# Performance work log

Hardware: AMD Instinct MI355X
Metric: run time of the kernel (lower is better)

Reference implementation:

```python
import jax, jax.numpy as jnp
import numpy as np


def _tet_geometry(vertices, indices, tet_density):
    """Gather 4 corners per tet, compute area (|det|/6), min edge length, alpha."""
    v = vertices[indices]                      # [T,4,3]
    v0, v1, v2, v3 = v[:, 0], v[:, 1], v[:, 2], v[:, 3]
    # --- tet area: |det([v1-v0, v2-v0, v3-v0])| / 6 ---
    e1, e2, e3 = v1 - v0, v2 - v0, v3 - v0     # [T,3] each
    det = (e1[:, 0] * (e2[:, 1] * e3[:, 2] - e2[:, 2] * e3[:, 1])
           - e1[:, 1] * (e2[:, 0] * e3[:, 2] - e2[:, 2] * e3[:, 0])
           + e1[:, 2] * (e2[:, 0] * e3[:, 1] - e2[:, 1] * e3[:, 0]))
    tet_area = jnp.abs(det) / 6.0              # [T]
    # --- edge lengths of all 6 edges, take min (mode='min') ---
    edge_sq = jnp.stack([
        jnp.sum((v0 - v1) ** 2, axis=1),
        jnp.sum((v0 - v2) ** 2, axis=1),
        jnp.sum((v0 - v3) ** 2, axis=1),
        jnp.sum((v1 - v2) ** 2, axis=1),
        jnp.sum((v1 - v3) ** 2, axis=1),
        jnp.sum((v2 - v3) ** 2, axis=1),
    ], axis=0)                                 # [6,T]
    el = jnp.sqrt(jnp.min(edge_sq, axis=0))    # [T]
    tet_alpha = 1.0 - jnp.exp(-tet_density * el)
    return tet_area, tet_alpha


def _vert_density(tet_density, indices, num_verts):
    # torch scatter_reduce_ 'amax' with zero-initialized dest and include_self=True
    # == segment_max over all 4 corner slots, clamped below at 0.
    flat_idx = indices.reshape(-1)                         # [4T]
    src = jnp.repeat(tet_density, 4)                       # [4T], matches row-major flatten
    vmax = jax.ops.segment_max(src, flat_idx, num_segments=num_verts)
    return jnp.maximum(vmax, jnp.zeros((), vmax.dtype))    # untouched verts -> 0


def setup_inputs() -> dict:
    key = jax.random.key(0)
    k1, k2, k3 = jax.random.split(key, 3)
    V, T = 1_000_000, 4_000_000
    vertices = jax.random.normal(k1, (V, 3), dtype=jnp.float32)
    indices = jax.random.randint(k2, (T, 4), 0, V, dtype=jnp.int32)
    tet_density = jax.random.uniform(k3, (T,), dtype=jnp.float32)
    return {"vertices": vertices, "indices": indices, "tet_density": tet_density}


def reference(vertices, indices, tet_density):
    tet_area, tet_alpha = _tet_geometry(vertices, indices, tet_density)
    vert_density = _vert_density(tet_density, indices, vertices.shape[0])
    return tet_area, tet_alpha, vert_density
```

## Files before the change

kernel.cpp:

```cpp
#include <hip/hip_runtime.h>

typedef int nt_int4 __attribute__((ext_vector_type(4)));

#define NB     256
#define VSHIFT 12
#define BMASK  ((1 << VSHIFT) - 1)
#define BCAP   65536
#define RT     4
#define NR     4

__global__ __launch_bounds__(256) void zero_kernel(uint4* __restrict__ vd4, int n4,
                                                   unsigned* __restrict__ gcnt) {
    int i = blockIdx.x * blockDim.x + threadIdx.x;
    if (i < n4) vd4[i] = make_uint4(0u, 0u, 0u, 0u);
    if (gcnt && i < NB) gcnt[i] = 0u;
}

__global__ __launch_bounds__(256) void pad_verts_kernel(const float* __restrict__ verts,
                                                        float4* __restrict__ verts4, int V) {
    int i = blockIdx.x * blockDim.x + threadIdx.x;
    if (i < V) {
        const float* p = verts + (size_t)i * 3;
        verts4[i] = make_float4(p[0], p[1], p[2], 0.f);
    }
}

__global__ __launch_bounds__(256) void geom_kernel_v4(
    const float4* __restrict__ verts4,
    const int*   __restrict__ indices,
    const float* __restrict__ density,
    float* __restrict__ out_area,
    float* __restrict__ out_alpha,
    int T)
{
    int i = blockIdx.x * blockDim.x + threadIdx.x;
    if (i >= T) return;

    nt_int4 idx = __builtin_nontemporal_load((const nt_int4*)indices + i);
    float d     = __builtin_nontemporal_load(&density[i]);

    float4 v0 = verts4[idx.x];
    float4 v1 = verts4[idx.y];
    float4 v2 = verts4[idx.z];
    float4 v3 = verts4[idx.w];

    float e1x = v1.x - v0.x, e1y = v1.y - v0.y, e1z = v1.z - v0.z;
    float e2x = v2.x - v0.x, e2y = v2.y - v0.y, e2z = v2.z - v0.z;
    float e3x = v3.x - v0.x, e3y = v3.y - v0.y, e3z = v3.z - v0.z;

    float det = e1x * (e2y * e3z - e2z * e3y)
              - e1y * (e2x * e3z - e2z * e3x)
              + e1z * (e2x * e3y - e2y * e3x);
    __builtin_nontemporal_store(fabsf(det) * (1.0f / 6.0f), &out_area[i]);

    float q01 = e1x * e1x + e1y * e1y + e1z * e1z;
    float q02 = e2x * e2x + e2y * e2y + e2z * e2z;
    float q03 = e3x * e3x + e3y * e3y + e3z * e3z;
    float ax, ay, az;
    ax = v1.x - v2.x; ay = v1.y - v2.y; az = v1.z - v2.z;
    float q12 = ax * ax + ay * ay + az * az;
    ax = v1.x - v3.x; ay = v1.y - v3.y; az = v1.z - v3.z;
    float q13 = ax * ax + ay * ay + az * az;
    ax = v2.x - v3.x; ay = v2.y - v3.y; az = v2.z - v3.z;
    float q23 = ax * ax + ay * ay + az * az;

    float mn = fminf(fminf(fminf(q01, q02), fminf(q03, q12)), fminf(q13, q23));
    float el = sqrtf(mn);
    __builtin_nontemporal_store(1.0f - expf(-d * el), &out_alpha[i]);
}

__global__ __launch_bounds__(256) void geom_kernel_raw(
    const float* __restrict__ verts,
    const int*   __restrict__ indices,
    const float* __restrict__ density,
    float* __restrict__ out_area,
    float* __restrict__ out_alpha,
    int T)
{
    int i = blockIdx.x * blockDim.x + threadIdx.x;
    if (i >= T) return;

    nt_int4 idx = __builtin_nontemporal_load((const nt_int4*)indices + i);
    float d     = __builtin_nontemporal_load(&density[i]);

    const float* p;
    p = verts + (size_t)idx.x * 3; float v0x = p[0], v0y = p[1], v0z = p[2];
    p = verts + (size_t)idx.y * 3; float v1x = p[0], v1y = p[1], v1z = p[2];
    p = verts + (size_t)idx.z * 3; float v2x = p[0], v2y = p[1], v2z = p[2];
    p = verts + (size_t)idx.w * 3; float v3x = p[0], v3y = p[1], v3z = p[2];

    float e1x = v1x - v0x, e1y = v1y - v0y, e1z = v1z - v0z;
    float e2x = v2x - v0x, e2y = v2y - v0y, e2z = v2z - v0z;
    float e3x = v3x - v0x, e3y = v3y - v0y, e3z = v3z - v0z;

    float det = e1x * (e2y * e3z - e2z * e3y)
              - e1y * (e2x * e3z - e2z * e3x)
              + e1z * (e2x * e3y - e2y * e3x);
    __builtin_nontemporal_store(fabsf(det) * (1.0f / 6.0f), &out_area[i]);

    float q01 = e1x * e1x + e1y * e1y + e1z * e1z;
    float q02 = e2x * e2x + e2y * e2y + e2z * e2z;
    float q03 = e3x * e3x + e3y * e3y + e3z * e3z;
    float ax, ay, az;
    ax = v1x - v2x; ay = v1y - v2y; az = v1z - v2z;
    float q12 = ax * ax + ay * ay + az * az;
    ax = v1x - v3x; ay = v1y - v3y; az = v1z - v3z;
    float q13 = ax * ax + ay * ay + az * az;
    ax = v2x - v3x; ay = v2y - v3y; az = v2z - v3z;
    float q23 = ax * ax + ay * ay + az * az;

    float mn = fminf(fminf(fminf(q01, q02), fminf(q03, q12)), fminf(q13, q23));
    float el = sqrtf(mn);
    __builtin_nontemporal_store(1.0f - expf(-d * el), &out_alpha[i]);
}

__global__ __launch_bounds__(256) void bin2_kernel(
    const int4*  __restrict__ idx4,
    const float* __restrict__ dens,
    uint2*       __restrict__ pairs,
    unsigned*    __restrict__ gcnt,
    unsigned*    __restrict__ vd,
    int T)
{
    __shared__ unsigned s_cnt[NB];
    __shared__ unsigned s_run[NB];
    __shared__ unsigned s_roff[NB];
    __shared__ unsigned s_wc[NB];
    __shared__ unsigned s_scan[NB];
    __shared__ uint2    stage[256 * RT * 4];

    int tid  = threadIdx.x;
    int base = blockIdx.x * (256 * RT * NR);

    s_cnt[tid] = 0u;
    __syncthreads();
    for (int k = 0; k < RT * NR; ++k) {
        int i = base + k * 256 + tid;
        if (i < T) {
            int4 q = idx4[i];
            atomicAdd(&s_cnt[(unsigned)q.x >> VSHIFT], 1u);
            atomicAdd(&s_cnt[(unsigned)q.y >> VSHIFT], 1u);
            atomicAdd(&s_cnt[(unsigned)q.z >> VSHIFT], 1u);
            atomicAdd(&s_cnt[(unsigned)q.w >> VSHIFT], 1u);
        }
    }
    __syncthreads();

    s_run[tid] = atomicAdd(&gcnt[tid], s_cnt[tid]);
    __syncthreads();

    for (int r = 0; r < NR; ++r) {
        int4  q[RT];
        float dd[RT];
        bool  vl[RT];
#pragma unroll
        for (int k = 0; k < RT; ++k) {
            int i = base + (r * RT + k) * 256 + tid;
            vl[k] = (i < T);
            if (vl[k]) { q[k] = idx4[i]; dd[k] = dens[i]; }
        }

        s_cnt[tid] = 0u;
        __syncthreads();
#pragma unroll
        for (int k = 0; k < RT; ++k) if (vl[k]) {
            atomicAdd(&s_cnt[(unsigned)q[k].x >> VSHIFT], 1u);
            atomicAdd(&s_cnt[(unsigned)q[k].y >> VSHIFT], 1u);
            atomicAdd(&s_cnt[(unsigned)q[k].z >> VSHIFT], 1u);
            atomicAdd(&s_cnt[(unsigned)q[k].w >> VSHIFT], 1u);
        }
        __syncthreads();

        unsigned x = s_cnt[tid];
        s_scan[tid] = x;
        __syncthreads();
        for (int s = 1; s < NB; s <<= 1) {
            unsigned t = (tid >= s) ? s_scan[tid - s] : 0u;
            __syncthreads();
            s_scan[tid] += t;
            __syncthreads();
        }
        s_roff[tid] = s_scan[tid] - x;
        s_wc[tid]   = 0u;
        __syncthreads();
        unsigned npairs = s_scan[NB - 1];

#pragma unroll
        for (int k = 0; k < RT; ++k) if (vl[k]) {
            unsigned db = __float_as_uint(dd[k]);
            unsigned vv[4] = { (unsigned)q[k].x, (unsigned)q[k].y,
                               (unsigned)q[k].z, (unsigned)q[k].w };
#pragma unroll
            for (int j = 0; j < 4; ++j) {
                unsigned b    = vv[j] >> VSHIFT;
                unsigned slot = s_roff[b] + atomicAdd(&s_wc[b], 1u);
                stage[slot] = make_uint2(vv[j], db);
            }
        }
        __syncthreads();

        for (unsigned l = tid; l < npairs; l += 256) {
            uint2 e = stage[l];
            unsigned b  = e.x >> VSHIFT;
            unsigned rr = s_run[b] + (l - s_roff[b]);
            if (rr < BCAP) pairs[(size_t)b * BCAP + rr] = e;
            else           atomicMax(vd + e.x, e.y);
        }
        __syncthreads();

        s_run[tid] += s_cnt[tid];
        __syncthreads();
    }
}

__global__ __launch_bounds__(1024) void bucket_max_kernel(
    const uint2*    __restrict__ pairs,
    const unsigned* __restrict__ gcnt,
    unsigned*       __restrict__ vd,
    int V)
{
    __shared__ unsigned tbl[1 << VSHIFT];
    int b   = blockIdx.x;
    int tid = threadIdx.x;

    for (int j = tid; j < (1 << VSHIFT); j += 1024) tbl[j] = 0u;
    __syncthreads();

    unsigned cnt = gcnt[b];
    if (cnt > BCAP) cnt = BCAP;
    const uint2* p = pairs + (size_t)b * BCAP;
    for (unsigned i = tid; i < cnt; i += 1024) {
        uint2 e = p[i];
        atomicMax(&tbl[e.x & BMASK], e.y);
    }
    __syncthreads();

    int vbase = b << VSHIFT;
    for (int j = tid; j < (1 << VSHIFT); j += 1024) {
        int v = vbase + j;
        if (v < V) {
            unsigned cur = vd[v];
            unsigned t   = tbl[j];
            vd[v] = cur > t ? cur : t;
        }
    }
}

__global__ __launch_bounds__(256) void tet_kernel_filter(
    const float4* __restrict__ verts4,
    const int*   __restrict__ indices,
    const float* __restrict__ density,
    float* __restrict__ out_area,
    float* __restrict__ out_alpha,
    unsigned int* __restrict__ vd,
    int T)
{
    int i = blockIdx.x * blockDim.x + threadIdx.x;
    if (i >= T) return;

    nt_int4 idx = __builtin_nontemporal_load((const nt_int4*)indices + i);
    float d     = __builtin_nontemporal_load(&density[i]);
    unsigned int db = __float_as_uint(d);

    unsigned int c0 = vd[idx.x];
    unsigned int c1 = vd[idx.y];
    unsigned int c2 = vd[idx.z];
    unsigned int c3 = vd[idx.w];

    float4 v0 = verts4[idx.x];
    float4 v1 = verts4[idx.y];
    float4 v2 = verts4[idx.z];
    float4 v3 = verts4[idx.w];

    float e1x = v1.x - v0.x, e1y = v1.y - v0.y, e1z = v1.z - v0.z;
    float e2x = v2.x - v0.x, e2y = v2.y - v0.y, e2z = v2.z - v0.z;
    float e3x = v3.x - v0.x, e3y = v3.y - v0.y, e3z = v3.z - v0.z;

    float det = e1x * (e2y * e3z - e2z * e3y)
              - e1y * (e2x * e3z - e2z * e3x)
              + e1z * (e2x * e3y - e2y * e3x);
    __builtin_nontemporal_store(fabsf(det) * (1.0f / 6.0f), &out_area[i]);

    float q01 = e1x * e1x + e1y * e1y + e1z * e1z;
    float q02 = e2x * e2x + e2y * e2y + e2z * e2z;
    float q03 = e3x * e3x + e3y * e3y + e3z * e3z;
    float ax, ay, az;
    ax = v1.x - v2.x; ay = v1.y - v2.y; az = v1.z - v2.z;
    float q12 = ax * ax + ay * ay + az * az;
    ax = v1.x - v3.x; ay = v1.y - v3.y; az = v1.z - v3.z;
    float q13 = ax * ax + ay * ay + az * az;
    ax = v2.x - v3.x; ay = v2.y - v3.y; az = v2.z - v3.z;
    float q23 = ax * ax + ay * ay + az * az;

    float mn = fminf(fminf(fminf(q01, q02), fminf(q03, q12)), fminf(q13, q23));
    float el = sqrtf(mn);
    __builtin_nontemporal_store(1.0f - expf(-d * el), &out_alpha[i]);

    if (db > c0) atomicMax(vd + idx.x, db);
    if (db > c1) atomicMax(vd + idx.y, db);
    if (db > c2) atomicMax(vd + idx.z, db);
    if (db > c3) atomicMax(vd + idx.w, db);
}

__global__ __launch_bounds__(256) void tet_kernel_fb(
    const float* __restrict__ verts,
    const int4*  __restrict__ indices,
    const float* __restrict__ density,
    float* __restrict__ out_area,
    float* __restrict__ out_alpha,
    unsigned int* __restrict__ vd,
    int T)
{
    int i = blockIdx.x * blockDim.x + threadIdx.x;
    if (i >= T) return;

    int4 idx = indices[i];
    float d = density[i];

    const float* p;
    p = verts + idx.x * 3; float v0x = p[0], v0y = p[1], v0z = p[2];
    p = verts + idx.y * 3; float v1x = p[0], v1y = p[1], v1z = p[2];
    p = verts + idx.z * 3; float v2x = p[0], v2y = p[1], v2z = p[2];
    p = verts + idx.w * 3; float v3x = p[0], v3y = p[1], v3z = p[2];

    float e1x = v1x - v0x, e1y = v1y - v0y, e1z = v1z - v0z;
    float e2x = v2x - v0x, e2y = v2y - v0y, e2z = v2z - v0z;
    float e3x = v3x - v0x, e3y = v3y - v0y, e3z = v3z - v0z;

    float det = e1x * (e2y * e3z - e2z * e3y)
              - e1y * (e2x * e3z - e2z * e3x)
              + e1z * (e2x * e3y - e2y * e3x);
    out_area[i] = fabsf(det) * (1.0f / 6.0f);

    float q01 = e1x * e1x + e1y * e1y + e1z * e1z;
    float q02 = e2x * e2x + e2y * e2y + e2z * e2z;
    float q03 = e3x * e3x + e3y * e3y + e3z * e3z;
    float ax, ay, az;
    ax = v1x - v2x; ay = v1y - v2y; az = v1z - v2z;
    float q12 = ax * ax + ay * ay + az * az;
    ax = v1x - v3x; ay = v1y - v3y; az = v1z - v3z;
    float q13 = ax * ax + ay * ay + az * az;
    ax = v2x - v3x; ay = v2y - v3y; az = v2z - v3z;
    float q23 = ax * ax + ay * ay + az * az;

    float mn = fminf(fminf(fminf(q01, q02), fminf(q03, q12)), fminf(q13, q23));
    float el = sqrtf(mn);
    out_alpha[i] = 1.0f - expf(-d * el);

    unsigned int db = __float_as_uint(d);
    atomicMax(vd + idx.x, db);
    atomicMax(vd + idx.y, db);
    atomicMax(vd + idx.z, db);
    atomicMax(vd + idx.w, db);
}


extern "C" void kernel_launch(void* const* d_in, const int* in_sizes, int n_in,
                              void* d_out, int out_size, void* d_ws, size_t ws_size,
                              hipStream_t stream) {
    const float* verts   = (const float*)d_in[0];
    const int*   indices = (const int*)d_in[1];
    const float* density = (const float*)d_in[2];
    int T = in_sizes[2];
    int V = in_sizes[0] / 3;

    float* out       = (float*)d_out;
    float* out_area  = out;
    float* out_alpha = out + (size_t)T;
    unsigned int* vd = (unsigned int*)(out + 2 * (size_t)T);

    const int block = 256;
    int n4 = V / 4;

    size_t pairsB = (size_t)NB * BCAP * sizeof(uint2);
    size_t cntB   = (size_t)NB * sizeof(unsigned);
    size_t v4B    = (size_t)V * sizeof(float4);

    double mean = 4.0 * (double)T / NB;
    bool capOK = (mean + 12.0 * __builtin_sqrt(mean) <= (double)BCAP);
    bool fastOK = (V % 4 == 0) && (V <= (NB << VSHIFT)) && capOK && d_ws;

    int tetsPerBlock = block * RT * NR;

    if (fastOK && ws_size >= pairsB + cntB + v4B) {
        uint2*    pairs  = (uint2*)d_ws;
        unsigned* gcnt   = (unsigned*)((char*)d_ws + pairsB);
        float4*   verts4 = (float4*)((char*)d_ws + pairsB + ((cntB + 255) & ~(size_t)255));

        zero_kernel<<<(n4 + block - 1) / block, block, 0, stream>>>((uint4*)vd, n4, gcnt);
        pad_verts_kernel<<<(V + block - 1) / block, block, 0, stream>>>(verts, verts4, V);
        geom_kernel_v4<<<(T + block - 1) / block, block, 0, stream>>>(
            verts4, indices, density, out_area, out_alpha, T);

        bin2_kernel<<<(T + tetsPerBlock - 1) / tetsPerBlock, block, 0, stream>>>(
            (const int4*)indices, density, pairs, gcnt, vd, T);

        int nbAct = (V + (1 << VSHIFT) - 1) >> VSHIFT;
        bucket_max_kernel<<<nbAct, 1024, 0, stream>>>(pairs, gcnt, vd, V);
    } else if (fastOK && ws_size >= pairsB + cntB) {
        uint2*    pairs = (uint2*)d_ws;
        unsigned* gcnt  = (unsigned*)((char*)d_ws + pairsB);

        zero_kernel<<<(n4 + block - 1) / block, block, 0, stream>>>((uint4*)vd, n4, gcnt);
        geom_kernel_raw<<<(T + block - 1) / block, block, 0, stream>>>(
            verts, indices, density, out_area, out_alpha, T);

        bin2_kernel<<<(T + tetsPerBlock - 1) / tetsPerBlock, block, 0, stream>>>(
            (const int4*)indices, density, pairs, gcnt, vd, T);

        int nbAct = (V + (1 << VSHIFT) - 1) >> VSHIFT;
        bucket_max_kernel<<<nbAct, 1024, 0, stream>>>(pairs, gcnt, vd, V);
    } else if (d_ws && ws_size >= v4B && (V % 4) == 0) {
        zero_kernel<<<(n4 + block - 1) / block, block, 0, stream>>>((uint4*)vd, n4, nullptr);
        float4* verts4 = (float4*)d_ws;
        pad_verts_kernel<<<(V + block - 1) / block, block, 0, stream>>>(verts, verts4, V);
        tet_kernel_filter<<<(T + block - 1) / block, block, 0, stream>>>(
            verts4, indices, density, out_area, out_alpha, vd, T);
    } else {
        zero_kernel<<<(n4 + block - 1) / block, block, 0, stream>>>((uint4*)vd, n4, nullptr);
        tet_kernel_fb<<<(T + block - 1) / block, block, 0, stream>>>(
            verts, (const int4*)indices, density, out_area, out_alpha, vd, T);
    }
}
```

Measured before the change: 450.0 us.

## Fuse tet geometry computation into the vertex-density binning kernel

The separate geometry kernel is removed, and its per-tet area and alpha computation now runs inside the binning kernel, reusing the index and density values that kernel already loads. This avoids reading the index and density arrays a second time and drops one launch. The fused kernel is launched with far fewer blocks (each handles 4096 tets) and has more register pressure, so the scattered vertex gathers may get less latency hiding. The fast path that lacked a padded-vertex workspace is also removed, so configurations that hit it now fall through to the filter or fallback paths.

Result: faster. 429.0 us (-4.7%).

```diff
diff --git a/kernel.cpp b/kernel.cpp
--- a/kernel.cpp
+++ b/kernel.cpp
@@ -25,98 +25,12 @@
     }
 }
 
-__global__ __launch_bounds__(256) void geom_kernel_v4(
+__global__ __launch_bounds__(256) void fused_geom_bin_kernel(
     const float4* __restrict__ verts4,
-    const int*   __restrict__ indices,
-    const float* __restrict__ density,
+    const int4*  __restrict__ idx4,
+    const float* __restrict__ dens,
     float* __restrict__ out_area,
     float* __restrict__ out_alpha,
-    int T)
-{
-    int i = blockIdx.x * blockDim.x + threadIdx.x;
-    if (i >= T) return;
-
-    nt_int4 idx = __builtin_nontemporal_load((const nt_int4*)indices + i);
-    float d     = __builtin_nontemporal_load(&density[i]);
-
-    float4 v0 = verts4[idx.x];
-    float4 v1 = verts4[idx.y];
-    float4 v2 = verts4[idx.z];
-    float4 v3 = verts4[idx.w];
-
-    float e1x = v1.x - v0.x, e1y = v1.y - v0.y, e1z = v1.z - v0.z;
-    float e2x = v2.x - v0.x, e2y = v2.y - v0.y, e2z = v2.z - v0.z;
-    float e3x = v3.x - v0.x, e3y = v3.y - v0.y, e3z = v3.z - v0.z;
-
-    float det = e1x * (e2y * e3z - e2z * e3y)
-              - e1y * (e2x * e3z - e2z * e3x)
-              + e1z * (e2x * e3y - e2y * e3x);
-    __builtin_nontemporal_store(fabsf(det) * (1.0f / 6.0f), &out_area[i]);
-
-    float q01 = e1x * e1x + e1y * e1y + e1z * e1z;
-    float q02 = e2x * e2x + e2y * e2y + e2z * e2z;
-    float q03 = e3x * e3x + e3y * e3y + e3z * e3z;
-    float ax, ay, az;
-    ax = v1.x - v2.x; ay = v1.y - v2.y; az = v1.z - v2.z;
-    float q12 = ax * ax + ay * ay + az * az;
-    ax = v1.x - v3.x; ay = v1.y - v3.y; az = v1.z - v3.z;
-    float q13 = ax * ax + ay * ay + az * az;
-    ax = v2.x - v3.x; ay = v2.y - v3.y; az = v2.z - v3.z;
-    float q23 = ax * ax + ay * ay + az * az;
-
-    float mn = fminf(fminf(fminf(q01, q02), fminf(q03, q12)), fminf(q13, q23));
-    float el = sqrtf(mn);
-    __builtin_nontemporal_store(1.0f - expf(-d * el), &out_alpha[i]);
-}
-
-__global__ __launch_bounds__(256) void geom_kernel_raw(
-    const float* __restrict__ verts,
-    const int*   __restrict__ indices,
-    const float* __restrict__ density,
-    float* __restrict__ out_area,
-    float* __restrict__ out_alpha,
-    int T)
-{
-    int i = blockIdx.x * blockDim.x + threadIdx.x;
-    if (i >= T) return;
-
-    nt_int4 idx = __builtin_nontemporal_load((const nt_int4*)indices + i);
-    float d     = __builtin_nontemporal_load(&density[i]);
-
-    const float* p;
-    p = verts + (size_t)idx.x * 3; float v0x = p[0], v0y = p[1], v0z = p[2];
-    p = verts + (size_t)idx.y * 3; float v1x = p[0], v1y = p[1], v1z = p[2];
-    p = verts + (size_t)idx.z * 3; float v2x = p[0], v2y = p[1], v2z = p[2];
-    p = verts + (size_t)idx.w * 3; float v3x = p[0], v3y = p[1], v3z = p[2];
-
-    float e1x = v1x - v0x, e1y = v1y - v0y, e1z = v1z - v0z;
-    float e2x = v2x - v0x, e2y = v2y - v0y, e2z = v2z - v0z;
-    float e3x = v3x - v0x, e3y = v3y - v0y, e3z = v3z - v0z;
-
-    float det = e1x * (e2y * e3z - e2z * e3y)
-              - e1y * (e2x * e3z - e2z * e3x)
-              + e1z * (e2x * e3y - e2y * e3x);
-    __builtin_nontemporal_store(fabsf(det) * (1.0f / 6.0f), &out_area[i]);
-
-    float q01 = e1x * e1x + e1y * e1y + e1z * e1z;
-    float q02 = e2x * e2x + e2y * e2y + e2z * e2z;
-    float q03 = e3x * e3x + e3y * e3y + e3z * e3z;
-    float ax, ay, az;
-    ax = v1x - v2x; ay = v1y - v2y; az = v1z - v2z;
-    float q12 = ax * ax + ay * ay + az * az;
-    ax = v1x - v3x; ay = v1y - v3y; az = v1z - v3z;
-    float q13 = ax * ax + ay * ay + az * az;
-    ax = v2x - v3x; ay = v2y - v3y; az = v2z - v3z;
-    float q23 = ax * ax + ay * ay + az * az;
-
-    float mn = fminf(fminf(fminf(q01, q02), fminf(q03, q12)), fminf(q13, q23));
-    float el = sqrtf(mn);
-    __builtin_nontemporal_store(1.0f - expf(-d * el), &out_alpha[i]);
-}
-
-__global__ __launch_bounds__(256) void bin2_kernel(
-    const int4*  __restrict__ idx4,
-    const float* __restrict__ dens,
     uint2*       __restrict__ pairs,
     unsigned*    __restrict__ gcnt,
     unsigned*    __restrict__ vd,
@@ -160,6 +74,39 @@
             if (vl[k]) { q[k] = idx4[i]; dd[k] = dens[i]; }
         }
 
+#pragma unroll
+        for (int k = 0; k < RT; ++k) if (vl[k]) {
+            int i = base + (r * RT + k) * 256 + tid;
+            float4 v0 = verts4[q[k].x];
+            float4 v1 = verts4[q[k].y];
+            float4 v2 = verts4[q[k].z];
+            float4 v3 = verts4[q[k].w];
+
+            float e1x = v1.x - v0.x, e1y = v1.y - v0.y, e1z = v1.z - v0.z;
+            float e2x = v2.x - v0.x, e2y = v2.y - v0.y, e2z = v2.z - v0.z;
+            float e3x = v3.x - v0.x, e3y = v3.y - v0.y, e3z = v3.z - v0.z;
+
+            float det = e1x * (e2y * e3z - e2z * e3y)
+                      - e1y * (e2x * e3z - e2z * e3x)
+                      + e1z * (e2x * e3y - e2y * e3x);
+            __builtin_nontemporal_store(fabsf(det) * (1.0f / 6.0f), &out_area[i]);
+
+            float q01 = e1x * e1x + e1y * e1y + e1z * e1z;
+            float q02 = e2x * e2x + e2y * e2y + e2z * e2z;
+            float q03 = e3x * e3x + e3y * e3y + e3z * e3z;
+            float ax, ay, az;
+            ax = v1.x - v2.x; ay = v1.y - v2.y; az = v1.z - v2.z;
+            float q12 = ax * ax + ay * ay + az * az;
+            ax = v1.x - v3.x; ay = v1.y - v3.y; az = v1.z - v3.z;
+            float q13 = ax * ax + ay * ay + az * az;
+            ax = v2.x - v3.x; ay = v2.y - v3.y; az = v2.z - v3.z;
+            float q23 = ax * ax + ay * ay + az * az;
+
+            float mn = fminf(fminf(fminf(q01, q02), fminf(q03, q12)), fminf(q13, q23));
+            float el = sqrtf(mn);
+            __builtin_nontemporal_store(1.0f - expf(-dd[k] * el), &out_alpha[i]);
+        }
+
         s_cnt[tid] = 0u;
         __syncthreads();
 #pragma unroll
@@ -381,6 +328,7 @@
     bool fastOK = (V % 4 == 0) && (V <= (NB << VSHIFT)) && capOK && d_ws;
 
     int tetsPerBlock = block * RT * NR;
+    int nbAct = (V + (1 << VSHIFT) - 1) >> VSHIFT;
 
     if (fastOK && ws_size >= pairsB + cntB + v4B) {
         uint2*    pairs  = (uint2*)d_ws;
@@ -389,26 +337,10 @@
 
         zero_kernel<<<(n4 + block - 1) / block, block, 0, stream>>>((uint4*)vd, n4, gcnt);
         pad_verts_kernel<<<(V + block - 1) / block, block, 0, stream>>>(verts, verts4, V);
-        geom_kernel_v4<<<(T + block - 1) / block, block, 0, stream>>>(
-            verts4, indices, density, out_area, out_alpha, T);
-
-        bin2_kernel<<<(T + tetsPerBlock - 1) / tetsPerBlock, block, 0, stream>>>(
-            (const int4*)indices, density, pairs, gcnt, vd, T);
-
-        int nbAct = (V + (1 << VSHIFT) - 1) >> VSHIFT;
-        bucket_max_kernel<<<nbAct, 1024, 0, stream>>>(pairs, gcnt, vd, V);
-    } else if (fastOK && ws_size >= pairsB + cntB) {
-        uint2*    pairs = (uint2*)d_ws;
-        unsigned* gcnt  = (unsigned*)((char*)d_ws + pairsB);
-
-        zero_kernel<<<(n4 + block - 1) / block, block, 0, stream>>>((uint4*)vd, n4, gcnt);
-        geom_kernel_raw<<<(T + block - 1) / block, block, 0, stream>>>(
-            verts, indices, density, out_area, out_alpha, T);
-
-        bin2_kernel<<<(T + tetsPerBlock - 1) / tetsPerBlock, block, 0, stream>>>(
-            (const int4*)indices, density, pairs, gcnt, vd, T);
-
-        int nbAct = (V + (1 << VSHIFT) - 1) >> VSHIFT;
+
+        fused_geom_bin_kernel<<<(T + tetsPerBlock - 1) / tetsPerBlock, block, 0, stream>>>(
+            verts4, (const int4*)indices, density, out_area, out_alpha, pairs, gcnt, vd, T);
+
         bucket_max_kernel<<<nbAct, 1024, 0, stream>>>(pairs, gcnt, vd, V);
     } else if (d_ws && ws_size >= v4B && (V % 4) == 0) {
         zero_kernel<<<(n4 + block - 1) / block, block, 0, stream>>>((uint4*)vd, n4, nullptr);
```
